# Kernel optimization log

Measured on AMD Instinct MI355X. Metric: run time of the kernel, lower is better.

## Reference

```python
import jax, jax.numpy as jnp
import numpy as np

B, S, E, H = 2, 2048, 1024, 16
D = E // H
LN_EPS = 1e-5
NORM_EPS = 1e-12  # F.normalize clamp_min


def setup_inputs() -> dict:
    key = jax.random.key(0)
    ks = jax.random.split(key, 4)
    x = jax.random.normal(ks[0], (B, S, E), dtype=jnp.float32)
    qkv_w = jax.random.normal(ks[1], (3 * E, E), dtype=jnp.float32) * 0.02
    qkv_b = jnp.zeros((3 * E,), dtype=jnp.float32)
    out_w = jax.random.normal(ks[2], (E, E), dtype=jnp.float32) * 0.02
    out_b = jnp.zeros((E,), dtype=jnp.float32)
    ln_w = jnp.ones((E,), dtype=jnp.float32)
    ln_b = jnp.zeros((E,), dtype=jnp.float32)
    qknorm_scale = jnp.asarray(E ** -0.5, dtype=jnp.float32)
    # RotaryEmbedding buffer: inv_freq interleaved (emb[::2] = emb[1::2] = base**(-arange(0,E,2)/E))
    base_freq = 10000.0 ** (-(np.arange(0, E, 2).astype(np.float32) / E))
    emb = np.empty((E,), dtype=np.float32)
    emb[::2] = base_freq
    emb[1::2] = base_freq
    inv_freq = jnp.asarray(emb)
    return {"x": x, "ln_w": ln_w, "ln_b": ln_b, "qkv_w": qkv_w, "qkv_b": qkv_b,
            "qknorm_scale": qknorm_scale, "out_w": out_w, "out_b": out_b, "inv_freq": inv_freq}


def _rotate(t, sin, cos):
    # Faithful to source: x1 = even idx (excluding last), x2 = odd idx; cat(-x2, x1)
    x1 = t[..., :-1:2]
    x2 = t[..., 1::2]
    t_rot = jnp.concatenate((-x2, x1), axis=-1)
    return t * cos + t_rot * sin


def _l2norm(t):
    n = jnp.sqrt(jnp.sum(t * t, axis=-1, keepdims=True))
    return t / jnp.maximum(n, NORM_EPS)


def reference(x, ln_w, ln_b, qkv_w, qkv_b, qknorm_scale, out_w, out_b, inv_freq):
    # --- prenorm (LayerNorm, eps=1e-5) ---
    mu = jnp.mean(x, axis=-1, keepdims=True)
    var = jnp.mean((x - mu) ** 2, axis=-1, keepdims=True)
    xn = (x - mu) / jnp.sqrt(var + LN_EPS) * ln_w + ln_b
    # --- QKV projection ---
    qkv = xn @ qkv_w.T + qkv_b  # [B,S,3E]
    q, k, v = jnp.split(qkv, 3, axis=-1)
    # --- rotary (source uses scalar seq*inv_freq, not per-position) ---
    seq = q.shape[1]
    sin = jnp.sin(seq * inv_freq)
    cos = jnp.cos(seq * inv_freq)
    q = _rotate(q, sin, cos)
    k = _rotate(k, sin, cos)
    # --- split heads: [B,S,E] -> [B,H,S,D] ---
    split = lambda t: t.reshape(B, seq, H, D).transpose(0, 2, 1, 3)
    q, k, v = split(q), split(k), split(v)
    # --- qknorm ---
    q = _l2norm(q) * qknorm_scale
    k = _l2norm(k) * qknorm_scale
    # --- scaled dot product with causal mask ---
    aw = jnp.einsum('bhqd,bhkd->bhqk', q, k)  # [B,H,S,S]
    causal = jnp.tril(jnp.ones((seq, seq), dtype=bool))
    aw = jnp.where(causal, aw, jnp.finfo(aw.dtype).min)
    aw = jax.nn.softmax(aw, axis=-1)
    attn = jnp.einsum('bhqk,bhkd->bhqd', aw, v)
    # --- merge heads + out proj ---
    attn = attn.transpose(0, 2, 1, 3).reshape(B, seq, E)
    return attn @ out_w.T + out_b
```

## Files before the change

### kernel.cpp

```cpp
#include <hip/hip_runtime.h>

typedef unsigned short u16;
typedef __attribute__((ext_vector_type(8))) short bf16x8;
typedef __attribute__((ext_vector_type(4))) float f32x4;

#define SS 2048
#define EE 1024
#define HH 16
#define DD 64

__device__ __forceinline__ float b2f(u16 u) {
  union { unsigned int i; float f; } v; v.i = ((unsigned int)u) << 16; return v.f;
}
__device__ __forceinline__ u16 f2b(float f) {
  union { float f; unsigned int i; } v; v.f = f;
  unsigned int i = v.i;
  return (u16)((i + 0x7FFFu + ((i >> 16) & 1u)) >> 16);
}
__device__ __forceinline__ unsigned int cvt_pk_bf16(float lo, float hi) {
  unsigned int r;
  asm("v_cvt_pk_bf16_f32 %0, %1, %2" : "=v"(r) : "v"(lo), "v"(hi));
  return r;
}

#define GLD16(g, l)                                                         \
  __builtin_amdgcn_global_load_lds(                                         \
      (const __attribute__((address_space(1))) unsigned int*)(g),           \
      (__attribute__((address_space(3))) unsigned int*)(l), 16, 0, 0)

__global__ __launch_bounds__(256) void k_prep(const float* __restrict__ qkv_w,
                                              u16* __restrict__ wq_b,
                                              const float* __restrict__ inv_freq,
                                              float2* __restrict__ cs,
                                              const float* __restrict__ x,
                                              const float* __restrict__ lw,
                                              const float* __restrict__ lb,
                                              u16* __restrict__ xn) {
  const int bx = blockIdx.x, t = threadIdx.x;
  if (bx < 3072) {
    const int i = bx * 256 + t;
    float4 v = ((const float4*)qkv_w)[i];
    ushort4 o;
    o.x = f2b(v.x); o.y = f2b(v.y); o.z = f2b(v.z); o.w = f2b(v.w);
    ((ushort4*)wq_b)[i] = o;
    return;
  }
  if (bx < 3076) {
    const int i = (bx - 3072) * 256 + t;
    float th = 2048.0f * inv_freq[i];
    cs[i] = make_float2(cosf(th), sinf(th));
    return;
  }
  const int row = bx - 3076;
  float4 v = ((const float4*)(x + (size_t)row * EE))[t];
  float f0 = v.x, f1 = v.y, f2 = v.z, f3 = v.w;
  float s = f0 + f1 + f2 + f3;
  float ss = f0 * f0 + f1 * f1 + f2 * f2 + f3 * f3;
  for (int o = 1; o < 64; o <<= 1) { s += __shfl_xor(s, o); ss += __shfl_xor(ss, o); }
  __shared__ float red[8];
  int w = t >> 6;
  if ((t & 63) == 0) { red[w] = s; red[4 + w] = ss; }
  __syncthreads();
  s = red[0] + red[1] + red[2] + red[3];
  ss = red[4] + red[5] + red[6] + red[7];
  float mu = s * (1.0f / 1024.0f);
  float var = ss * (1.0f / 1024.0f) - mu * mu;
  float rstd = rsqrtf(var + 1e-5f);
  float4 wv = ((const float4*)lw)[t];
  float4 bv = ((const float4*)lb)[t];
  ushort4 o;
  o.x = f2b((f0 - mu) * rstd * wv.x + bv.x);
  o.y = f2b((f1 - mu) * rstd * wv.y + bv.y);
  o.z = f2b((f2 - mu) * rstd * wv.z + bv.z);
  o.w = f2b((f3 - mu) * rstd * wv.w + bv.w);
  ((ushort4*)(xn + (size_t)row * EE))[t] = o;
}

__global__ __launch_bounds__(256) void k_gemm_b(const u16* __restrict__ A,
                                                const u16* __restrict__ W,
                                                const float* __restrict__ bias,
                                                u16* __restrict__ C,
                                                int M, int N, int K) {
  __shared__ __align__(16) u16 As[128 * 32];
  __shared__ __align__(16) u16 Ws[128 * 32];
  const int t = threadIdx.x;
  const int m0 = blockIdx.y * 128, n0 = blockIdx.x * 128;
  const int lane = t & 63, w = t >> 6, quad = lane >> 4, l15 = lane & 15;
  const int wm = (w & 1) * 64, wn = (w >> 1) * 64;

  f32x4 zero4 = {0.f, 0.f, 0.f, 0.f};
  f32x4 acc[4][4];
  for (int mi = 0; mi < 4; mi++)
    for (int ni = 0; ni < 4; ni++) acc[mi][ni] = zero4;

  const u16* Ag = A + (size_t)(m0 + (t >> 2)) * K + (t & 3) * 8;
  const u16* Wg = W + (size_t)(n0 + (t >> 2)) * K + (t & 3) * 8;
  const size_t rowskip = (size_t)64 * K;

  for (int k0 = 0; k0 < K; k0 += 32) {
    GLD16(Ag + k0, As + t * 8);
    GLD16(Ag + rowskip + k0, As + 2048 + t * 8);
    GLD16(Wg + k0, Ws + t * 8);
    GLD16(Wg + rowskip + k0, Ws + 2048 + t * 8);
    __syncthreads();
    bf16x8 af[4], wf[4];
#pragma unroll
    for (int i = 0; i < 4; i++) {
      af[i] = *(const bf16x8*)(As + (wm + i * 16 + l15) * 32 + quad * 8);
      wf[i] = *(const bf16x8*)(Ws + (wn + i * 16 + l15) * 32 + quad * 8);
    }
#pragma unroll
    for (int mi = 0; mi < 4; mi++)
#pragma unroll
      for (int ni = 0; ni < 4; ni++)
        acc[mi][ni] = __builtin_amdgcn_mfma_f32_16x16x32_bf16(af[mi], wf[ni], acc[mi][ni], 0, 0, 0);
    __syncthreads();
  }
  for (int mi = 0; mi < 4; mi++)
    for (int ni = 0; ni < 4; ni++) {
      int col = n0 + wn + ni * 16 + l15;
      float bb = bias[col];
      for (int r = 0; r < 4; r++) {
        int grow = m0 + wm + mi * 16 + quad * 4 + r;
        C[(size_t)grow * N + col] = f2b(acc[mi][ni][r] + bb);
      }
    }
}

__global__ __launch_bounds__(256) void k_gemm_fw(const u16* __restrict__ A,
                                                 const float* __restrict__ W,
                                                 const float* __restrict__ bias,
                                                 float* __restrict__ C,
                                                 int M, int N, int K) {
  __shared__ __align__(16) u16 As[64 * 32];
  __shared__ __align__(16) u16 Ws[128 * 32];
  const int t = threadIdx.x;
  const int m0 = blockIdx.y * 64, n0 = blockIdx.x * 128;
  const int lane = t & 63, w = t >> 6, quad = lane >> 4, l15 = lane & 15;
  const int wm = (w & 1) * 32, wn = (w >> 1) * 64;

  f32x4 zero4 = {0.f, 0.f, 0.f, 0.f};
  f32x4 acc[2][4];
  for (int mi = 0; mi < 2; mi++)
    for (int ni = 0; ni < 4; ni++) acc[mi][ni] = zero4;

  const u16* Ag = A + (size_t)(m0 + (t >> 2)) * K + (t & 3) * 8;
  const float* Wg0 = W + (size_t)(n0 + (t >> 2)) * K + (t & 3) * 8;
  const float* Wg1 = Wg0 + (size_t)64 * K;

  for (int k0 = 0; k0 < K; k0 += 32) {
    GLD16(Ag + k0, As + t * 8);
    float4 wa = *(const float4*)(Wg0 + k0);
    float4 wb = *(const float4*)(Wg0 + k0 + 4);
    float4 wc = *(const float4*)(Wg1 + k0);
    float4 wd = *(const float4*)(Wg1 + k0 + 4);
    union { unsigned int u[4]; bf16x8 v8; } p0, p1;
    p0.u[0] = cvt_pk_bf16(wa.x, wa.y); p0.u[1] = cvt_pk_bf16(wa.z, wa.w);
    p0.u[2] = cvt_pk_bf16(wb.x, wb.y); p0.u[3] = cvt_pk_bf16(wb.z, wb.w);
    p1.u[0] = cvt_pk_bf16(wc.x, wc.y); p1.u[1] = cvt_pk_bf16(wc.z, wc.w);
    p1.u[2] = cvt_pk_bf16(wd.x, wd.y); p1.u[3] = cvt_pk_bf16(wd.z, wd.w);
    *(bf16x8*)(Ws + t * 8) = p0.v8;
    *(bf16x8*)(Ws + 2048 + t * 8) = p1.v8;
    __syncthreads();
    bf16x8 af[2], wf[4];
#pragma unroll
    for (int i = 0; i < 2; i++)
      af[i] = *(const bf16x8*)(As + (wm + i * 16 + l15) * 32 + quad * 8);
#pragma unroll
    for (int i = 0; i < 4; i++)
      wf[i] = *(const bf16x8*)(Ws + (wn + i * 16 + l15) * 32 + quad * 8);
#pragma unroll
    for (int mi = 0; mi < 2; mi++)
#pragma unroll
      for (int ni = 0; ni < 4; ni++)
        acc[mi][ni] = __builtin_amdgcn_mfma_f32_16x16x32_bf16(af[mi], wf[ni], acc[mi][ni], 0, 0, 0);
    __syncthreads();
  }
  for (int mi = 0; mi < 2; mi++)
    for (int ni = 0; ni < 4; ni++) {
      int col = n0 + wn + ni * 16 + l15;
      float bb = bias[col];
      for (int r = 0; r < 4; r++) {
        int grow = m0 + wm + mi * 16 + quad * 4 + r;
        C[(size_t)grow * N + col] = acc[mi][ni][r] + bb;
      }
    }
}

__global__ __launch_bounds__(256) void k_rotv(u16* __restrict__ qkv,
                                              const float2* __restrict__ cs_tab,
                                              const float* __restrict__ scale_p,
                                              u16* __restrict__ vt) {
  __shared__ float qf[1024];
  __shared__ float kf[1024];
  __shared__ __align__(16) u16 tile[64 * 72];
  const int row = blockIdx.x, t = threadIdx.x;
  {
    u16* qr = qkv + (size_t)row * 3072;
    u16* kr = qr + 1024;
    ushort4 qv = ((const ushort4*)qr)[t];
    ushort4 kv = ((const ushort4*)kr)[t];
    *(float4*)(qf + 4 * t) = make_float4(b2f(qv.x), b2f(qv.y), b2f(qv.z), b2f(qv.w));
    *(float4*)(kf + 4 * t) = make_float4(b2f(kv.x), b2f(kv.y), b2f(kv.z), b2f(kv.w));
    __syncthreads();
    const float scale = scale_p[0];
    float rq[4], rk[4];
#pragma unroll
    for (int u = 0; u < 4; u++) {
      int j = 4 * t + u;
      float2 cs = cs_tab[j];
      float qrot = (j < 512) ? -qf[2 * j + 1] : qf[2 * (j - 512)];
      float krot = (j < 512) ? -kf[2 * j + 1] : kf[2 * (j - 512)];
      rq[u] = qf[j] * cs.x + qrot * cs.y;
      rk[u] = kf[j] * cs.x + krot * cs.y;
    }
    float ssq = rq[0] * rq[0] + rq[1] * rq[1] + rq[2] * rq[2] + rq[3] * rq[3];
    float ssk = rk[0] * rk[0] + rk[1] * rk[1] + rk[2] * rk[2] + rk[3] * rk[3];
    for (int o = 1; o < 16; o <<= 1) { ssq += __shfl_xor(ssq, o); ssk += __shfl_xor(ssk, o); }
    float qs = scale / fmaxf(sqrtf(ssq), 1e-12f);
    float ks = scale / fmaxf(sqrtf(ssk), 1e-12f);
    ushort4 qo, ko;
    qo.x = f2b(rq[0] * qs); qo.y = f2b(rq[1] * qs); qo.z = f2b(rq[2] * qs); qo.w = f2b(rq[3] * qs);
    ko.x = f2b(rk[0] * ks); ko.y = f2b(rk[1] * ks); ko.z = f2b(rk[2] * ks); ko.w = f2b(rk[3] * ks);
    ((ushort4*)qr)[t] = qo;
    ((ushort4*)kr)[t] = ko;
  }
  if (row >= 1024) return;
  const int st = row & 31, bh = row >> 5;
  const int b = bh >> 4, h = bh & 15;
  const int s0 = st * 64;
  const int si = t >> 2, dc = t & 3;
  __syncthreads();
  const u16* src = qkv + (size_t)(b * SS + s0 + si) * 3072 + 2048 + h * DD;
  bf16x8 v0 = *(const bf16x8*)(src + dc * 8);
  bf16x8 v1 = *(const bf16x8*)(src + (dc + 4) * 8);
#pragma unroll
  for (int u = 0; u < 8; u++) tile[(dc * 8 + u) * 72 + si] = (u16)v0[u];
#pragma unroll
  for (int u = 0; u < 8; u++) tile[((dc + 4) * 8 + u) * 72 + si] = (u16)v1[u];
  __syncthreads();
#pragma unroll
  for (int it = 0; it < 2; it++) {
    int idx = t + it * 256;
    int d = idx >> 3, ch = idx & 7;
    bf16x8 o = *(const bf16x8*)(tile + d * 72 + ch * 8);
    *(bf16x8*)(vt + (size_t)(bh * DD + d) * SS + s0 + ch * 8) = o;
  }
}

__global__ __launch_bounds__(512) void k_attn(const u16* __restrict__ qkv,
                                              const u16* __restrict__ vt,
                                              u16* __restrict__ out) {
  __shared__ __align__(16) u16 Kt[128 * 72];
  __shared__ __align__(16) u16 Vt[64 * 136];
  __shared__ __align__(16) u16 Pt[128 * 136];
  const int bh = blockIdx.y;
  const int b = bh >> 4, h = bh & 15;
  const int t = threadIdx.x, w = t >> 6, lane = t & 63, quad = lane >> 4, l15 = lane & 15;
  const int krow = t >> 2, kq = (t & 3) * 16;
  const int dr = t >> 3, kc8 = t & 7;
  const int srcl = (lane & 48) + ((lane >> 4) << 2);
  const u16* kn = qkv + 1024;
  f32x4 zero4 = {0.f, 0.f, 0.f, 0.f};

  for (int rep = 0; rep < 2; rep++) {
    const int qt = rep ? 15 - (int)blockIdx.x : (int)blockIdx.x;
    const int q0 = qt * 128;

    bf16x8 qf[2];
    {
      const u16* qrow = qkv + (size_t)(b * SS + q0 + 16 * w + l15) * 3072 + h * DD;
      qf[0] = *(const bf16x8*)(qrow + quad * 8);
      qf[1] = *(const bf16x8*)(qrow + 32 + quad * 8);
    }
    f32x4 oacc[4];
    for (int n = 0; n < 4; n++) oacc[n] = zero4;
    float m_i = -1e30f, l_i = 0.f;

    bf16x8 kv[2], vv[2];
    {
      const u16* krg = kn + (size_t)(b * SS + krow) * 3072 + h * DD + kq;
      kv[0] = *(const bf16x8*)(krg);
      kv[1] = *(const bf16x8*)(krg + 8);
      const u16* vrg = vt + (size_t)(bh * DD + dr) * SS + kc8 * 16;
      vv[0] = *(const bf16x8*)(vrg);
      vv[1] = *(const bf16x8*)(vrg + 8);
    }
    __syncthreads();
    *(bf16x8*)(Kt + krow * 72 + kq) = kv[0];
    *(bf16x8*)(Kt + krow * 72 + kq + 8) = kv[1];
    *(bf16x8*)(Vt + dr * 136 + kc8 * 16) = vv[0];
    *(bf16x8*)(Vt + dr * 136 + kc8 * 16 + 8) = vv[1];
    __syncthreads();

    for (int kt = 0; kt <= qt; kt++) {
      if (kt < qt) {
        const int k0n = (kt + 1) * 128;
        const u16* krg = kn + (size_t)(b * SS + k0n + krow) * 3072 + h * DD + kq;
        kv[0] = *(const bf16x8*)(krg);
        kv[1] = *(const bf16x8*)(krg + 8);
        const u16* vrg = vt + (size_t)(bh * DD + dr) * SS + k0n + kc8 * 16;
        vv[0] = *(const bf16x8*)(vrg);
        vv[1] = *(const bf16x8*)(vrg + 8);
      }
      f32x4 sacc[8];
#pragma unroll
      for (int n = 0; n < 8; n++) {
        sacc[n] = zero4;
#pragma unroll
        for (int c = 0; c < 2; c++) {
          bf16x8 kfrag = *(const bf16x8*)(Kt + (n * 16 + l15) * 72 + c * 32 + quad * 8);
          sacc[n] = __builtin_amdgcn_mfma_f32_16x16x32_bf16(kfrag, qf[c], sacc[n], 0, 0, 0);
        }
      }
      if (kt == qt) {
        const int qrow = 16 * w + l15, kbase = 4 * quad;
#pragma unroll
        for (int n = 0; n < 8; n++)
#pragma unroll
          for (int r = 0; r < 4; r++)
            if (16 * n + kbase + r > qrow) sacc[n][r] = -1e30f;
      }
      float mx = -1e30f;
#pragma unroll
      for (int n = 0; n < 8; n++)
#pragma unroll
        for (int r = 0; r < 4; r++) mx = fmaxf(mx, sacc[n][r]);
      mx = fmaxf(mx, __shfl_xor(mx, 16));
      mx = fmaxf(mx, __shfl_xor(mx, 32));
      float mn = fmaxf(m_i, mx);
      float al = __expf(m_i - mn);
      m_i = mn;
      float rs = 0.f;
#pragma unroll
      for (int n = 0; n < 8; n++)
#pragma unroll
        for (int r = 0; r < 4; r++) {
          float p = __expf(sacc[n][r] - mn);
          sacc[n][r] = p;
          rs += p;
        }
      rs += __shfl_xor(rs, 16);
      rs += __shfl_xor(rs, 32);
      l_i = al * l_i + rs;
      float alr[4];
#pragma unroll
      for (int r = 0; r < 4; r++) alr[r] = __shfl(al, srcl + r);
#pragma unroll
      for (int n = 0; n < 4; n++)
#pragma unroll
        for (int r = 0; r < 4; r++) oacc[n][r] *= alr[r];
#pragma unroll
      for (int n = 0; n < 8; n++) {
        uint2 pk;
        pk.x = cvt_pk_bf16(sacc[n][0], sacc[n][1]);
        pk.y = cvt_pk_bf16(sacc[n][2], sacc[n][3]);
        *(uint2*)(Pt + (16 * w + l15) * 136 + 16 * n + 4 * quad) = pk;
      }
      __syncthreads();
#pragma unroll
      for (int c = 0; c < 4; c++) {
        bf16x8 pf = *(const bf16x8*)(Pt + (16 * w + l15) * 136 + c * 32 + quad * 8);
#pragma unroll
        for (int n = 0; n < 4; n++) {
          bf16x8 vf = *(const bf16x8*)(Vt + (n * 16 + l15) * 136 + c * 32 + quad * 8);
          oacc[n] = __builtin_amdgcn_mfma_f32_16x16x32_bf16(pf, vf, oacc[n], 0, 0, 0);
        }
      }
      __syncthreads();
      if (kt < qt) {
        *(bf16x8*)(Kt + krow * 72 + kq) = kv[0];
        *(bf16x8*)(Kt + krow * 72 + kq + 8) = kv[1];
        *(bf16x8*)(Vt + dr * 136 + kc8 * 16) = vv[0];
        *(bf16x8*)(Vt + dr * 136 + kc8 * 16 + 8) = vv[1];
      }
      __syncthreads();
    }
    float lr[4];
#pragma unroll
    for (int r = 0; r < 4; r++) lr[r] = __shfl(l_i, srcl + r);
    for (int n = 0; n < 4; n++)
      for (int r = 0; r < 4; r++) {
        int row = q0 + 16 * w + quad * 4 + r;
        out[(size_t)(b * SS + row) * EE + h * DD + n * 16 + l15] = f2b(oacc[n][r] / lr[r]);
      }
  }
}

extern "C" void kernel_launch(void* const* d_in, const int* in_sizes, int n_in,
                              void* d_out, int out_size, void* d_ws, size_t ws_size,
                              hipStream_t stream) {
  const float* x       = (const float*)d_in[0];
  const float* ln_w    = (const float*)d_in[1];
  const float* ln_b    = (const float*)d_in[2];
  const float* qkv_w   = (const float*)d_in[3];
  const float* qkv_b   = (const float*)d_in[4];
  const float* qk_s    = (const float*)d_in[5];
  const float* out_w   = (const float*)d_in[6];
  const float* out_b   = (const float*)d_in[7];
  const float* inv_frq = (const float*)d_in[8];

  u16* ws   = (u16*)d_ws;
  u16* xn   = ws;
  u16* qkv  = ws + (size_t)4096 * 1024;
  u16* wq_b = (u16*)d_out;
  float2* cs_tab = (float2*)((char*)d_out + 6291456);
  u16* vt   = (u16*)d_out + (size_t)4194304;

  k_prep<<<7172, 256, 0, stream>>>(qkv_w, wq_b, inv_frq, cs_tab, x, ln_w, ln_b, xn);
  k_gemm_b<<<dim3(24, 32), 256, 0, stream>>>(xn, wq_b, qkv_b, qkv, 4096, 3072, 1024);
  k_rotv<<<4096, 256, 0, stream>>>(qkv, cs_tab, qk_s, vt);
  k_attn<<<dim3(8, 32), 512, 0, stream>>>(qkv, vt, xn);
  k_gemm_fw<<<dim3(8, 64), 256, 0, stream>>>(xn, out_w, out_b, (float*)d_out, 4096, 1024, 1024);
}
```

Before: 219.0 us.

## Double-buffer K/V tiles in attention, drop barriers, and swizzle GEMM block order

The attention kernel now keeps two LDS buffers for K and V. The next tile is written into the idle buffer while the current one is consumed, which cuts the per-iteration barriers from three to one. The P-tile barrier becomes a local lgkmcnt wait, since each wave reads only its own P rows. Both GEMM kernels also remap workgroup IDs with an XCD-style stride-8 swizzle for better cache locality. The extra K/V buffers raise LDS use, and the swizzle assumes the block count divides by 8.

```diff
diff --git a/kernel.cpp b/kernel.cpp
--- a/kernel.cpp
+++ b/kernel.cpp
@@ -84,7 +84,10 @@
   __shared__ __align__(16) u16 As[128 * 32];
   __shared__ __align__(16) u16 Ws[128 * 32];
   const int t = threadIdx.x;
-  const int m0 = blockIdx.y * 128, n0 = blockIdx.x * 128;
+  const int flat = blockIdx.y * gridDim.x + blockIdx.x;
+  const int nwg8 = (int)(gridDim.x * gridDim.y) >> 3;
+  const int sw = (flat & 7) * nwg8 + (flat >> 3);
+  const int m0 = (sw / (int)gridDim.x) * 128, n0 = (sw % (int)gridDim.x) * 128;
   const int lane = t & 63, w = t >> 6, quad = lane >> 4, l15 = lane & 15;
   const int wm = (w & 1) * 64, wn = (w >> 1) * 64;
 
@@ -135,7 +138,10 @@
   __shared__ __align__(16) u16 As[64 * 32];
   __shared__ __align__(16) u16 Ws[128 * 32];
   const int t = threadIdx.x;
-  const int m0 = blockIdx.y * 64, n0 = blockIdx.x * 128;
+  const int flat = blockIdx.y * gridDim.x + blockIdx.x;
+  const int nwg8 = (int)(gridDim.x * gridDim.y) >> 3;
+  const int sw = (flat & 7) * nwg8 + (flat >> 3);
+  const int m0 = (sw / (int)gridDim.x) * 64, n0 = (sw % (int)gridDim.x) * 128;
   const int lane = t & 63, w = t >> 6, quad = lane >> 4, l15 = lane & 15;
   const int wm = (w & 1) * 32, wn = (w >> 1) * 64;
 
@@ -251,8 +257,8 @@
 __global__ __launch_bounds__(512) void k_attn(const u16* __restrict__ qkv,
                                               const u16* __restrict__ vt,
                                               u16* __restrict__ out) {
-  __shared__ __align__(16) u16 Kt[128 * 72];
-  __shared__ __align__(16) u16 Vt[64 * 136];
+  __shared__ __align__(16) u16 Kt[2][128 * 72];
+  __shared__ __align__(16) u16 Vt[2][64 * 136];
   __shared__ __align__(16) u16 Pt[128 * 136];
   const int bh = blockIdx.y;
   const int b = bh >> 4, h = bh & 15;
@@ -287,11 +293,12 @@
       vv[1] = *(const bf16x8*)(vrg + 8);
     }
     __syncthreads();
-    *(bf16x8*)(Kt + krow * 72 + kq) = kv[0];
-    *(bf16x8*)(Kt + krow * 72 + kq + 8) = kv[1];
-    *(bf16x8*)(Vt + dr * 136 + kc8 * 16) = vv[0];
-    *(bf16x8*)(Vt + dr * 136 + kc8 * 16 + 8) = vv[1];
-    __syncthreads();
+    *(bf16x8*)(Kt[0] + krow * 72 + kq) = kv[0];
+    *(bf16x8*)(Kt[0] + krow * 72 + kq + 8) = kv[1];
+    *(bf16x8*)(Vt[0] + dr * 136 + kc8 * 16) = vv[0];
+    *(bf16x8*)(Vt[0] + dr * 136 + kc8 * 16 + 8) = vv[1];
+    __syncthreads();
+    int cur = 0;
 
     for (int kt = 0; kt <= qt; kt++) {
       if (kt < qt) {
@@ -303,13 +310,15 @@
         vv[0] = *(const bf16x8*)(vrg);
         vv[1] = *(const bf16x8*)(vrg + 8);
       }
+      const u16* Kc = Kt[cur];
+      const u16* Vc = Vt[cur];
       f32x4 sacc[8];
 #pragma unroll
       for (int n = 0; n < 8; n++) {
         sacc[n] = zero4;
 #pragma unroll
         for (int c = 0; c < 2; c++) {
-          bf16x8 kfrag = *(const bf16x8*)(Kt + (n * 16 + l15) * 72 + c * 32 + quad * 8);
+          bf16x8 kfrag = *(const bf16x8*)(Kc + (n * 16 + l15) * 72 + c * 32 + quad * 8);
           sacc[n] = __builtin_amdgcn_mfma_f32_16x16x32_bf16(kfrag, qf[c], sacc[n], 0, 0, 0);
         }
       }
@@ -357,24 +366,25 @@
         pk.y = cvt_pk_bf16(sacc[n][2], sacc[n][3]);
         *(uint2*)(Pt + (16 * w + l15) * 136 + 16 * n + 4 * quad) = pk;
       }
-      __syncthreads();
+      asm volatile("s_waitcnt lgkmcnt(0)" ::: "memory");
+      __builtin_amdgcn_sched_barrier(0);
 #pragma unroll
       for (int c = 0; c < 4; c++) {
         bf16x8 pf = *(const bf16x8*)(Pt + (16 * w + l15) * 136 + c * 32 + quad * 8);
 #pragma unroll
         for (int n = 0; n < 4; n++) {
-          bf16x8 vf = *(const bf16x8*)(Vt + (n * 16 + l15) * 136 + c * 32 + quad * 8);
+          bf16x8 vf = *(const bf16x8*)(Vc + (n * 16 + l15) * 136 + c * 32 + quad * 8);
           oacc[n] = __builtin_amdgcn_mfma_f32_16x16x32_bf16(pf, vf, oacc[n], 0, 0, 0);
         }
       }
+      if (kt < qt) {
+        *(bf16x8*)(Kt[cur ^ 1] + krow * 72 + kq) = kv[0];
+        *(bf16x8*)(Kt[cur ^ 1] + krow * 72 + kq + 8) = kv[1];
+        *(bf16x8*)(Vt[cur ^ 1] + dr * 136 + kc8 * 16) = vv[0];
+        *(bf16x8*)(Vt[cur ^ 1] + dr * 136 + kc8 * 16 + 8) = vv[1];
+      }
       __syncthreads();
-      if (kt < qt) {
-        *(bf16x8*)(Kt + krow * 72 + kq) = kv[0];
-        *(bf16x8*)(Kt + krow * 72 + kq + 8) = kv[1];
-        *(bf16x8*)(Vt + dr * 136 + kc8 * 16) = vv[0];
-        *(bf16x8*)(Vt + dr * 136 + kc8 * 16 + 8) = vv[1];
-      }
-      __syncthreads();
+      cur ^= 1;
     }
     float lr[4];
 #pragma unroll
```

After: 216.3 us. Within noise of the previous version (-1.2%).
